# Performance work log

Hardware: AMD Instinct MI355X
Metric: run time of the kernel (lower is better)

The kernel has to match this reference:

```python
import jax, jax.numpy as jnp
import numpy as np

N = 8192
K = 16  # k neighbors; layer uses k+1 columns

def setup_inputs() -> dict:
    key = jax.random.key(0)
    k1, k2 = jax.random.split(key)
    data_input = jax.random.normal(k1, (N, N), dtype=jnp.float32)
    neighbor_indices = jax.random.randint(k2, (N, K + 1), 0, N, dtype=jnp.int64)
    return {"data_input": data_input, "neighbor_indices": neighbor_indices}

def reference(data_input, neighbor_indices):
    # Original builds a sparse (n,n) adjacency with ones at (i, Idx[i,j]),
    # multiplies elementwise with dense data_input, then row-sums.
    # Equivalent (including duplicate-index accumulation) to gathering each
    # row's k+1 neighbor scores and summing them.
    idx = neighbor_indices[:, : K + 1]                 # (n, k+1)
    gathered = jnp.take_along_axis(data_input, idx, axis=1)  # (n, k+1)
    A_raw = jnp.sum(gathered, axis=1)                  # (n,)
    alpha = jax.nn.softmax(A_raw)                      # (n,)
    return (alpha, A_raw)
```

## Files before the change

### kernel.cpp

```cpp
#include <hip/hip_runtime.h>
#include <math.h>

#define NROWS 8192
#define KP1   17

__global__ __launch_bounds__(512) void gather_sum_kernel(
    const float* __restrict__ data,
    const int* __restrict__ nidx,
    float* __restrict__ a_raw)
{
    int tid = blockIdx.x * 512 + threadIdx.x;
    int row = tid >> 4;
    int k   = tid & 15;

    const int* ip = nidx + row * KP1;
    int c0  = ip[k];
    int c16 = ip[16];

    const float* rp = data + (size_t)row * NROWS;
    float v   = rp[c0];
    float v16 = rp[c16];

    v += (k == 0) ? v16 : 0.0f;

    #pragma unroll
    for (int off = 8; off > 0; off >>= 1)
        v += __shfl_down(v, off, 16);

    if (k == 0) a_raw[row] = v;
}

__global__ __launch_bounds__(1024) void softmax_norm_kernel(
    const float* __restrict__ a_raw,
    float* __restrict__ alpha)
{
    __shared__ float red[16];
    const int t    = threadIdx.x;
    const int wave = t >> 6;
    const int lane = t & 63;

    float vals[8];
    float s = 0.0f;
    #pragma unroll
    for (int i = 0; i < 8; ++i) {
        vals[i] = expf(a_raw[t + i * 1024]);
        s += vals[i];
    }
    #pragma unroll
    for (int off = 32; off > 0; off >>= 1)
        s += __shfl_down(s, off, 64);
    if (lane == 0) red[wave] = s;
    __syncthreads();
    if (wave == 0) {
        float ss = (lane < 16) ? red[lane] : 0.0f;
        #pragma unroll
        for (int off = 8; off > 0; off >>= 1)
            ss += __shfl_down(ss, off, 64);
        if (lane == 0) red[0] = ss;
    }
    __syncthreads();
    const float inv = 1.0f / red[0];

    float mine = vals[0];
    #pragma unroll
    for (int i = 1; i < 8; ++i)
        if ((int)blockIdx.x == i) mine = vals[i];

    alpha[blockIdx.x * 1024 + t] = mine * inv;
}

extern "C" void kernel_launch(void* const* d_in, const int* in_sizes, int n_in,
                              void* d_out, int out_size, void* d_ws, size_t ws_size,
                              hipStream_t stream) {
    const float* data = (const float*)d_in[0];
    const int*   nidx = (const int*)d_in[1];
    float* alpha = (float*)d_out;
    float* a_raw = (float*)d_out + NROWS;

    gather_sum_kernel<<<(NROWS * 16) / 512, 512, 0, stream>>>(data, nidx, a_raw);
    softmax_norm_kernel<<<8, 1024, 0, stream>>>(a_raw, alpha);
}
```

Baseline: 12.65 us.

## Fuse exp partial sums into gather kernel and shrink softmax kernel

The gather kernel now computes exp of each row sum and reduces a per-block partial sum into workspace. The softmax kernel then needs only 256 partial sums per block instead of having each block recompute all 8192 exponentials, and it launches 32 blocks of 256 threads. This removes redundant exp work and global reads in the second kernel, at the cost of a block-wide barrier and extra LDS traffic in the gather kernel. Like the original, it does no max subtraction.

```diff
diff --git a/kernel.cpp b/kernel.cpp
--- a/kernel.cpp
+++ b/kernel.cpp
@@ -3,13 +3,18 @@
 
 #define NROWS 8192
 #define KP1   17
+#define RPB_A 32
 
 __global__ __launch_bounds__(512) void gather_sum_kernel(
     const float* __restrict__ data,
     const int* __restrict__ nidx,
-    float* __restrict__ a_raw)
+    float* __restrict__ a_raw,
+    float* __restrict__ partial)
 {
-    int tid = blockIdx.x * 512 + threadIdx.x;
+    __shared__ float lds_exp[RPB_A];
+
+    const int t   = threadIdx.x;
+    int tid = blockIdx.x * 512 + t;
     int row = tid >> 4;
     int k   = tid & 15;
 
@@ -27,46 +32,44 @@
     for (int off = 8; off > 0; off >>= 1)
         v += __shfl_down(v, off, 16);
 
-    if (k == 0) a_raw[row] = v;
+    if (k == 0) {
+        a_raw[row] = v;
+        lds_exp[t >> 4] = expf(v);
+    }
+    __syncthreads();
+
+    if (t < 32) {
+        float p = lds_exp[t];
+        #pragma unroll
+        for (int off = 16; off > 0; off >>= 1)
+            p += __shfl_down(p, off, 32);
+        if (t == 0) partial[blockIdx.x] = p;
+    }
 }
 
-__global__ __launch_bounds__(1024) void softmax_norm_kernel(
+__global__ __launch_bounds__(256) void softmax_norm_kernel(
     const float* __restrict__ a_raw,
+    const float* __restrict__ partial,
     float* __restrict__ alpha)
 {
-    __shared__ float red[16];
+    __shared__ float red[4];
     const int t    = threadIdx.x;
     const int wave = t >> 6;
     const int lane = t & 63;
+    const int row  = blockIdx.x * 256 + t;
 
-    float vals[8];
-    float s = 0.0f;
-    #pragma unroll
-    for (int i = 0; i < 8; ++i) {
-        vals[i] = expf(a_raw[t + i * 1024]);
-        s += vals[i];
-    }
+    float e = expf(a_raw[row]);
+
+    float s = partial[t];
     #pragma unroll
     for (int off = 32; off > 0; off >>= 1)
         s += __shfl_down(s, off, 64);
     if (lane == 0) red[wave] = s;
     __syncthreads();
-    if (wave == 0) {
-        float ss = (lane < 16) ? red[lane] : 0.0f;
-        #pragma unroll
-        for (int off = 8; off > 0; off >>= 1)
-            ss += __shfl_down(ss, off, 64);
-        if (lane == 0) red[0] = ss;
-    }
+    if (t == 0) red[0] = (red[0] + red[1]) + (red[2] + red[3]);
     __syncthreads();
-    const float inv = 1.0f / red[0];
 
-    float mine = vals[0];
-    #pragma unroll
-    for (int i = 1; i < 8; ++i)
-        if ((int)blockIdx.x == i) mine = vals[i];
-
-    alpha[blockIdx.x * 1024 + t] = mine * inv;
+    alpha[row] = e * (1.0f / red[0]);
 }
 
 extern "C" void kernel_launch(void* const* d_in, const int* in_sizes, int n_in,
@@ -74,9 +77,10 @@
                               hipStream_t stream) {
     const float* data = (const float*)d_in[0];
     const int*   nidx = (const int*)d_in[1];
-    float* alpha = (float*)d_out;
-    float* a_raw = (float*)d_out + NROWS;
+    float* alpha   = (float*)d_out;
+    float* a_raw   = (float*)d_out + NROWS;
+    float* partial = (float*)d_ws;
 
-    gather_sum_kernel<<<(NROWS * 16) / 512, 512, 0, stream>>>(data, nidx, a_raw);
-    softmax_norm_kernel<<<8, 1024, 0, stream>>>(a_raw, alpha);
+    gather_sum_kernel<<<(NROWS * 16) / 512, 512, 0, stream>>>(data, nidx, a_raw, partial);
+    softmax_norm_kernel<<<32, 256, 0, stream>>>(a_raw, partial, alpha);
 }
```

Result: faster. 11.32 us (median of 2 runs) (-10.5%).
